# Kernel optimization log

Measured on AMD Instinct MI355X. Metric: run time of the kernel, lower is better.

## Reference

```python
import jax, jax.numpy as jnp
import numpy as np

RANK = 16
SHAPE = (512, 512, 512)


def setup_inputs() -> dict:
    key = jax.random.key(0)
    k0, k1, k2 = jax.random.split(key, 3)
    # factors initialized like torch.randn(rank, n_dim) / 100.0
    f0 = jax.random.normal(k0, (RANK, SHAPE[0]), dtype=jnp.float32) / 100.0
    f1 = jax.random.normal(k1, (RANK, SHAPE[1]), dtype=jnp.float32) / 100.0
    f2 = jax.random.normal(k2, (RANK, SHAPE[2]), dtype=jnp.float32) / 100.0
    return {"f0": f0, "f1": f1, "f2": f2}


def reference(f0, f1, f2):
    # CP/PARAFAC reconstruction: sum over rank of outer products.
    # Equivalent to torch.einsum('ka,kb,kc->abc', f0, f1, f2).
    # Expressed so XLA contracts (ka,kb->abk) via GEMM then (abk,kc->abc):
    return jnp.einsum('ka,kb,kc->abc', f0, f1, f2)
```

## Files before the change

### kernel.cpp

```cpp
#include <hip/hip_runtime.h>

#define RANK 16
#define N 512
#define BTILE 64
#define NBLK (N / BTILE)
#define NCHUNK (N * NBLK)
#define CPB 4
#define GRID (NCHUNK / CPB)

typedef float vfloat4 __attribute__((ext_vector_type(4)));

__global__ __launch_bounds__(256) void parafac_kernel(
    const float* __restrict__ f0,
    const float* __restrict__ f1,
    const float* __restrict__ f2,
    float* __restrict__ out)
{
    __shared__ float pt[RANK][BTILE];

    const int t    = threadIdx.x;
    const int wave = t >> 6;
    const int lane = t & 63;
    const int rbase = (wave >> 1) * 32;
    const int c4    = (wave & 1) * 256 + lane * 4;

    vfloat4 v[RANK];
#pragma unroll
    for (int k = 0; k < RANK; ++k)
        v[k] = *reinterpret_cast<const vfloat4*>(&f2[k * N + c4]);

    const int sk  = t >> 4;
    const int sbi = (t & 15) * 4;

    for (int ci = 0; ci < CPB; ++ci) {
        const int cid = blockIdx.x * CPB + ci;
        const int a   = cid / NBLK;
        const int b0  = (cid % NBLK) * BTILE;

        {
            const float s = f0[sk * N + a];
            const vfloat4 f1v = *reinterpret_cast<const vfloat4*>(&f1[sk * N + b0 + sbi]);
            *reinterpret_cast<vfloat4*>(&pt[sk][sbi]) = s * f1v;
        }
        __syncthreads();

        float* outa = out + ((size_t)a * N + b0) * N + c4;

#pragma unroll
        for (int it = 0; it < 8; ++it) {
            if (it != 0) __builtin_amdgcn_s_barrier();
            const int bb = rbase + it * 4;
            vfloat4 acc0 = (vfloat4)(0.f);
            vfloat4 acc1 = (vfloat4)(0.f);
            vfloat4 acc2 = (vfloat4)(0.f);
            vfloat4 acc3 = (vfloat4)(0.f);
#pragma unroll
            for (int k = 0; k < RANK; ++k) {
                const vfloat4 pk = *reinterpret_cast<const vfloat4*>(&pt[k][bb]);
                const vfloat4 vk = v[k];
                acc0 += pk.x * vk;
                acc1 += pk.y * vk;
                acc2 += pk.z * vk;
                acc3 += pk.w * vk;
            }
            float* o = outa + (size_t)bb * N;
            *reinterpret_cast<vfloat4*>(o)         = acc0;
            *reinterpret_cast<vfloat4*>(o + N)     = acc1;
            *reinterpret_cast<vfloat4*>(o + 2 * N) = acc2;
            *reinterpret_cast<vfloat4*>(o + 3 * N) = acc3;
        }
        __syncthreads();
    }
}

extern "C" void kernel_launch(void* const* d_in, const int* in_sizes, int n_in,
                              void* d_out, int out_size, void* d_ws, size_t ws_size,
                              hipStream_t stream) {
    const float* f0 = (const float*)d_in[0];
    const float* f1 = (const float*)d_in[1];
    const float* f2 = (const float*)d_in[2];
    float* out = (float*)d_out;

    dim3 grid(GRID);
    dim3 block(256);
    parafac_kernel<<<grid, block, 0, stream>>>(f0, f1, f2, out);
}
```

Baseline: 100.1 us.

## Transpose shared partial-product tile and interleave row assignment across waves

Stores the f0*f1 partial-product tile as [row][rank] rather than [rank][row], so each output row's 16 rank coefficients are read as four contiguous vector loads. Work is now split by interleaved pairs of rows between wave pairs instead of contiguous 32-row halves. This doubles the iteration count and the barriers per chunk. Each iteration keeps two accumulators instead of four, so both wave pairs write neighbouring rows at the same time. The staging step now does scalar global loads of f1 with four multiplies per thread instead of one vector load.

```diff
diff --git a/kernel.cpp b/kernel.cpp
--- a/kernel.cpp
+++ b/kernel.cpp
@@ -4,9 +4,8 @@
 #define N 512
 #define BTILE 64
 #define NBLK (N / BTILE)
-#define NCHUNK (N * NBLK)
 #define CPB 4
-#define GRID (NCHUNK / CPB)
+#define GRID (N * NBLK / CPB)
 
 typedef float vfloat4 __attribute__((ext_vector_type(4)));
 
@@ -16,12 +15,12 @@
     const float* __restrict__ f2,
     float* __restrict__ out)
 {
-    __shared__ float pt[RANK][BTILE];
+    __shared__ float pt[BTILE][RANK];
 
-    const int t    = threadIdx.x;
-    const int wave = t >> 6;
-    const int lane = t & 63;
-    const int rbase = (wave >> 1) * 32;
+    const int t     = threadIdx.x;
+    const int wave  = t >> 6;
+    const int lane  = t & 63;
+    const int wp2   = wave >> 1;
     const int c4    = (wave & 1) * 256 + lane * 4;
 
     vfloat4 v[RANK];
@@ -29,8 +28,8 @@
     for (int k = 0; k < RANK; ++k)
         v[k] = *reinterpret_cast<const vfloat4*>(&f2[k * N + c4]);
 
-    const int sk  = t >> 4;
-    const int sbi = (t & 15) * 4;
+    const int sr  = t & 63;
+    const int skq = (t >> 6) * 4;
 
     for (int ci = 0; ci < CPB; ++ci) {
         const int cid = blockIdx.x * CPB + ci;
@@ -38,36 +37,39 @@
         const int b0  = (cid % NBLK) * BTILE;
 
         {
-            const float s = f0[sk * N + a];
-            const vfloat4 f1v = *reinterpret_cast<const vfloat4*>(&f1[sk * N + b0 + sbi]);
-            *reinterpret_cast<vfloat4*>(&pt[sk][sbi]) = s * f1v;
+            vfloat4 w;
+#pragma unroll
+            for (int j = 0; j < 4; ++j) {
+                const int k = skq + j;
+                w[j] = f0[k * N + a] * f1[k * N + b0 + sr];
+            }
+            *reinterpret_cast<vfloat4*>(&pt[sr][skq]) = w;
         }
         __syncthreads();
 
         float* outa = out + ((size_t)a * N + b0) * N + c4;
 
 #pragma unroll
-        for (int it = 0; it < 8; ++it) {
+        for (int it = 0; it < BTILE / 4; ++it) {
             if (it != 0) __builtin_amdgcn_s_barrier();
-            const int bb = rbase + it * 4;
+            const int r0 = it * 4 + wp2 * 2;
+            const vfloat4* pr0 = reinterpret_cast<const vfloat4*>(&pt[r0][0]);
+            const vfloat4* pr1 = reinterpret_cast<const vfloat4*>(&pt[r0 + 1][0]);
             vfloat4 acc0 = (vfloat4)(0.f);
             vfloat4 acc1 = (vfloat4)(0.f);
-            vfloat4 acc2 = (vfloat4)(0.f);
-            vfloat4 acc3 = (vfloat4)(0.f);
 #pragma unroll
-            for (int k = 0; k < RANK; ++k) {
-                const vfloat4 pk = *reinterpret_cast<const vfloat4*>(&pt[k][bb]);
-                const vfloat4 vk = v[k];
-                acc0 += pk.x * vk;
-                acc1 += pk.y * vk;
-                acc2 += pk.z * vk;
-                acc3 += pk.w * vk;
+            for (int q = 0; q < 4; ++q) {
+                const vfloat4 p0 = pr0[q];
+                const vfloat4 p1 = pr1[q];
+#pragma unroll
+                for (int j = 0; j < 4; ++j) {
+                    acc0 += p0[j] * v[q * 4 + j];
+                    acc1 += p1[j] * v[q * 4 + j];
+                }
             }
-            float* o = outa + (size_t)bb * N;
-            *reinterpret_cast<vfloat4*>(o)         = acc0;
-            *reinterpret_cast<vfloat4*>(o + N)     = acc1;
-            *reinterpret_cast<vfloat4*>(o + 2 * N) = acc2;
-            *reinterpret_cast<vfloat4*>(o + 3 * N) = acc3;
+            float* o = outa + (size_t)r0 * N;
+            *reinterpret_cast<vfloat4*>(o)     = acc0;
+            *reinterpret_cast<vfloat4*>(o + N) = acc1;
         }
         __syncthreads();
     }
```

Measured after the change: 109.8 us. +9.7%, slower.
